# Optimization experiments

Hardware: AMD Instinct MI355X
Metric: run time of the kernel (lower is better)

## Reference

```python
import jax, jax.numpy as jnp
import numpy as np
from functools import partial

T, B, IN, H = 512, 32, 1024, 1024
NUM_LAYERS = 2
SLOPE, OFFSET = 0.2, 0.5
FORGET_GATE_BIAS = 1.0
W_SCALE = 1.0 / np.sqrt(H)  # mimics reset_parameters uniform(-1/sqrt(H), 1/sqrt(H)) scale


def setup_inputs() -> dict:
    key = jax.random.key(0)
    ks = jax.random.split(key, 12)
    x = jax.random.normal(ks[0], (T, B, IN), dtype=jnp.float32)
    h0 = jax.random.normal(ks[1], (NUM_LAYERS, B, H), dtype=jnp.float32)
    c0 = jax.random.normal(ks[2], (NUM_LAYERS, B, H), dtype=jnp.float32)
    def u(k, shape):
        return jax.random.uniform(k, shape, jnp.float32, -W_SCALE, W_SCALE)
    # layer 0: input_size=IN, layer 1: input_size=H
    W_ih0 = u(ks[3], (4 * H, IN))
    W_hh0 = u(ks[4], (4 * H, H))
    b_ih0 = u(ks[5], (4 * H,)).at[H:2 * H].set(FORGET_GATE_BIAS)
    b_hh0 = u(ks[6], (4 * H,)).at[H:2 * H].set(0.0)
    W_ih1 = u(ks[7], (4 * H, H))
    W_hh1 = u(ks[8], (4 * H, H))
    b_ih1 = u(ks[9], (4 * H,)).at[H:2 * H].set(FORGET_GATE_BIAS)
    b_hh1 = u(ks[10], (4 * H,)).at[H:2 * H].set(0.0)
    return {"x": x, "h0": h0, "c0": c0,
            "W_ih0": W_ih0, "W_hh0": W_hh0, "b_ih0": b_ih0, "b_hh0": b_hh0,
            "W_ih1": W_ih1, "W_hh1": W_hh1, "b_ih1": b_ih1, "b_hh1": b_hh1}


def _hard_sigmoid(g):
    return jnp.clip(SLOPE * g + OFFSET, 0.0, 1.0)


def _hardtanh(g):
    return jnp.clip(g, -1.0, 1.0)


def _run_layer(x, h, c, W_ih, W_hh, b_ih, b_hh):
    """HardLSTMLayerForward: per-step eps = mean(x_t) is added to input and state."""
    def step(carry, xt):
        h, c = carry
        eps = jnp.mean(xt)
        xi = xt + eps          # [B, in]
        hh = h + eps           # [B, H]
        cc = c + eps           # [B, H]
        gates = xi @ W_ih.T + b_ih + hh @ W_hh.T + b_hh  # [B, 4H]
        i_g = _hard_sigmoid(gates[:, :H])
        f_g = _hard_sigmoid(gates[:, H:2 * H])
        g_g = _hardtanh(gates[:, 2 * H:3 * H])
        o_g = _hard_sigmoid(gates[:, 3 * H:])
        cy = f_g * cc + i_g * g_g
        hy = o_g * _hardtanh(cy)
        return (hy, cy), hy
    (h, c), y = jax.lax.scan(step, (h, c), x)
    return y, h, c


def reference(x, h0, c0, W_ih0, W_hh0, b_ih0, b_hh0, W_ih1, W_hh1, b_ih1, b_hh1):
    out = x + 1.0  # StackedLSTM adds `one` to the input
    y0, h_0, c_0 = _run_layer(out, h0[0], c0[0], W_ih0, W_hh0, b_ih0, b_hh0)
    y1, h_1, c_1 = _run_layer(y0, h0[1], c0[1], W_ih1, W_hh1, b_ih1, b_hh1)
    hn = jnp.stack([h_0, h_1])  # [num_layers, B, H]
    cn = jnp.stack([c_0, c_1])
    return (y1, hn, cn)
```

## Files before the change

### kernel.cpp

```cpp
#include <hip/hip_runtime.h>
#include <cstdio>


#define T_STEPS 512
#define DEADLINE_TICKS 6000000ULL

typedef __bf16 bf16x8 __attribute__((ext_vector_type(8)));
typedef float  f32x4  __attribute__((ext_vector_type(4)));
typedef unsigned int u32x4 __attribute__((ext_vector_type(4)));
typedef unsigned long long u64;

#define AGLD(p)   __hip_atomic_load((p), __ATOMIC_RELAXED, __HIP_MEMORY_SCOPE_AGENT)
#define AGST(p,v) __hip_atomic_store((p), (v), __ATOMIC_RELAXED, __HIP_MEMORY_SCOPE_AGENT)
#define MFMA16 __builtin_amdgcn_mfma_f32_16x16x32_bf16

__device__ __forceinline__ u64 rtick(){ return __builtin_amdgcn_s_memrealtime(); }

__device__ __forceinline__ unsigned short f2bf(float f){
  union { float f; unsigned u; } v; v.f = f;
  unsigned r = v.u + 0x7FFFu + ((v.u >> 16) & 1u);
  return (unsigned short)(r >> 16);
}
__device__ __forceinline__ bf16x8 packbf(f32x4 a, f32x4 b){
  unsigned u0 = f2bf(a[0]) | ((unsigned)f2bf(a[1])<<16);
  unsigned u1 = f2bf(a[2]) | ((unsigned)f2bf(a[3])<<16);
  unsigned u2 = f2bf(b[0]) | ((unsigned)f2bf(b[1])<<16);
  unsigned u3 = f2bf(b[2]) | ((unsigned)f2bf(b[3])<<16);
  u32x4 cv = {u0,u1,u2,u3};
  return __builtin_bit_cast(bf16x8, cv);
}
__device__ __forceinline__ int fragOff(int row, int k8){
  return ((k8>>2)*2 + (row>>4))*1024 + ((row&15) | ((k8&3)<<4))*16;
}
__device__ __forceinline__ bf16x8 ld_frag_plain(const char* p){
  u32x4 v = *reinterpret_cast<const u32x4*>(p);
  return __builtin_bit_cast(bf16x8, v);
}
__device__ __forceinline__ bf16x8 lds_frag(const char* p){
  u32x4 v = *reinterpret_cast<const u32x4*>(p);
  return __builtin_bit_cast(bf16x8, v);
}

__device__ __forceinline__ void stage64k_c(const char* src, char* dst, int tid){
  const u32x4* s = reinterpret_cast<const u32x4*>(src) + tid;
  u32x4 r0 = s[0],    r1 = s[256],  r2 = s[512],  r3 = s[768];
  u32x4 r4 = s[1024], r5 = s[1280], r6 = s[1536], r7 = s[1792];
  u32x4 r8 = s[2048], r9 = s[2304], ra = s[2560], rb = s[2816];
  u32x4 rc = s[3072], rd = s[3328], re = s[3584], rf = s[3840];
  u32x4* d = (u32x4*)(dst + tid*16);
  d[0]=r0; d[256]=r1; d[512]=r2; d[768]=r3;
  d[1024]=r4; d[1280]=r5; d[1536]=r6; d[1792]=r7;
  d[2048]=r8; d[2304]=r9; d[2560]=ra; d[2816]=rb;
  d[3072]=rc; d[3328]=rd; d[3584]=re; d[3840]=rf;
}
__device__ __forceinline__ void stage64k_b(const char* src, char* dst, int tid){
  u32x4 r0,r1,r2,r3,r4,r5,r6,r7,r8,r9,ra,rb,rc,rd,re,rf;
  u64 a = (u64)(uintptr_t)src + (u64)tid*16;
  #define LD(reg, off) asm volatile("global_load_dwordx4 %0, %1, off sc0 sc1" \
                                    : "=v"(reg) : "v"(a + (off)) : "memory")
  LD(r0,0); LD(r1,4096); LD(r2,8192); LD(r3,12288);
  LD(r4,16384); LD(r5,20480); LD(r6,24576); LD(r7,28672);
  LD(r8,32768); LD(r9,36864); LD(ra,40960); LD(rb,45056);
  LD(rc,49152); LD(rd,53248); LD(re,57344); LD(rf,61440);
  #undef LD
  asm volatile("s_waitcnt vmcnt(0)" ::: "memory");
  u32x4* d = (u32x4*)(dst + tid*16);
  d[0]=r0; d[256]=r1; d[512]=r2; d[768]=r3;
  d[1024]=r4; d[1280]=r5; d[1536]=r6; d[1792]=r7;
  d[2048]=r8; d[2304]=r9; d[2560]=ra; d[2816]=rb;
  d[3072]=rc; d[3328]=rd; d[3584]=re; d[3840]=rf;
}

__device__ __forceinline__ void spin64(const unsigned short* f, unsigned tgt,
                                       int lane, u64 dl){
  if (lane < 8){
    u64 a = (u64)(uintptr_t)f + (u64)lane*16;
    while (true){
      u32x4 v;
      asm volatile("global_load_dwordx4 %0, %1, off sc0 sc1\n\ts_waitcnt vmcnt(0)"
                   : "=v"(v) : "v"(a) : "memory");
      bool ok = true;
      #pragma unroll
      for (int i=0;i<4;++i){
        unsigned u = v[i];
        ok = ok && ((u & 0xFFFFu) >= tgt) && ((u >> 16) >= tgt);
      }
      if (__all((int)ok)) break;
      if (rtick() > dl) break;
    }
  }
  asm volatile("" ::: "memory");
}


__global__ void prep_xfrag(const float* __restrict__ x, unsigned short* __restrict__ xf){
  int tid = blockIdx.x*256 + threadIdx.x;
  int k8 = tid & 127, row = (tid>>7)&31, t = tid>>12;
  const float* s = x + ((size_t)(t*32+row)*1024 + k8*8);
  f32x4 a = *reinterpret_cast<const f32x4*>(s);
  f32x4 b = *reinterpret_cast<const f32x4*>(s+4);
  f32x4 a1 = {a[0]+1.f,a[1]+1.f,a[2]+1.f,a[3]+1.f};
  f32x4 b1 = {b[0]+1.f,b[1]+1.f,b[2]+1.f,b[3]+1.f};
  bf16x8 v = packbf(a1,b1);
  *reinterpret_cast<bf16x8*>((char*)xf + (size_t)t*65536 + fragOff(row,k8)) = v;
}

__global__ void prep_hfrag(const float* __restrict__ h0, unsigned short* __restrict__ hf){
  int tid = blockIdx.x*256 + threadIdx.x;
  int k8 = tid & 127, row = (tid>>7)&31, L = tid>>12;
  const float* s = h0 + ((size_t)(L*32+row)*1024 + k8*8);
  f32x4 a = *reinterpret_cast<const f32x4*>(s);
  f32x4 b = *reinterpret_cast<const f32x4*>(s+4);
  bf16x8 v = packbf(a,b);
  *reinterpret_cast<bf16x8*>((char*)hf + (size_t)L*65536 + fragOff(row,k8)) = v;
}

__global__ void reduce_mean_f32(const float* __restrict__ src, float* __restrict__ out, float add){
  __shared__ float red[256];
  int t = blockIdx.x, tid = threadIdx.x;
  const float* p = src + (size_t)t*32768;
  float s = 0.f;
  for (int i = tid; i < 32768; i += 256) s += p[i];
  red[tid] = s; __syncthreads();
  for (int o = 128; o > 0; o >>= 1){ if (tid < o) red[tid] += red[tid+o]; __syncthreads(); }
  if (tid == 0) out[t] = red[0]*(1.f/32768.f) + add;
}

__global__ void prep_rs(const float* __restrict__ Wih0, const float* __restrict__ Whh0,
                        const float* __restrict__ Wih1, const float* __restrict__ Whh1,
                        const float* __restrict__ bih0, const float* __restrict__ bhh0,
                        const float* __restrict__ bih1, const float* __restrict__ bhh1,
                        float* __restrict__ rs, float* __restrict__ bias){
  int task = blockIdx.x*4 + (threadIdx.x >> 6);
  int lane = threadIdx.x & 63;
  int L = task >> 12, n = task & 4095;
  const float* pi = (L ? Wih1 : Wih0) + (size_t)n*1024;
  const float* ph = (L ? Whh1 : Whh0) + (size_t)n*1024;
  float s = 0.f;
  #pragma unroll
  for (int e = 0; e < 16; ++e){ int k = lane + e*64; s += pi[k] + ph[k]; }
  #pragma unroll
  for (int m = 32; m; m >>= 1) s += __shfl_xor(s, m);
  if (lane == 0){
    rs[task]   = s;
    bias[task] = (L ? bih1[n] : bih0[n]) + (L ? bhh1[n] : bhh0[n]);
  }
}

__global__ __launch_bounds__(256, 1) void rec11(
    const unsigned short* __restrict__ Xf,
    const unsigned short* __restrict__ HiniF,
    unsigned short* __restrict__ Ring0,
    unsigned short* __restrict__ Ring1,
    int ring1mask, int ring1cached,
    float* __restrict__ out,
    const float* __restrict__ Wih0, const float* __restrict__ Whh0,
    const float* __restrict__ Wih1, const float* __restrict__ Whh1,
    const float* __restrict__ biasC, const float* __restrict__ rsC,
    const float* __restrict__ eps0, const float* __restrict__ c0,
    int* __restrict__ epsP,
    unsigned short* __restrict__ flag0,
    unsigned short* __restrict__ flag1)
{
  __shared__ char ldsA[65536];
  __shared__ float ldsPs[4];

  const int tid  = threadIdx.x;
  const int lane = tid & 63;
  const int w    = tid >> 6;
  const int L    = blockIdx.x >> 6;
  const int bid  = blockIdx.x & 63;
  const int jb   = bid * 16;
  const int jc   = jb + w*4;
  const int c    = lane & 15;
  const int q    = c >> 2;
  const int ncol = q*1024 + jc + (c & 3);
  const int koff = (lane >> 4) << 3;
  const u64 dl   = rtick() + DEADLINE_TICKS;

  __builtin_amdgcn_fence(__ATOMIC_ACQUIRE, "agent");
  __syncthreads();

  const float* Wfirst = L ? Whh1 : Wih0;
  const float* Wsec   = L ? Wih1 : Whh0;

  bf16x8 wregF[32], wregS[32];
  {
    const float* sF = Wfirst + (size_t)ncol*1024 + koff;
    const float* sS = Wsec   + (size_t)ncol*1024 + koff;
    #pragma unroll
    for (int kt = 0; kt < 32; ++kt){
      f32x4 a = *reinterpret_cast<const f32x4*>(sF + kt*32);
      f32x4 b = *reinterpret_cast<const f32x4*>(sF + kt*32 + 4);
      wregF[kt] = packbf(a, b);
      f32x4 cc = *reinterpret_cast<const f32x4*>(sS + kt*32);
      f32x4 d  = *reinterpret_cast<const f32x4*>(sS + kt*32 + 4);
      wregS[kt] = packbf(cc, d);
    }
  }

  const float bia = biasC[L*4096 + ncol];
  const float rsv = rsC[L*4096 + ncol];
  const int jw = jc + (c & 3);
  float creg[2][4];
  #pragma unroll
  for (int m = 0; m < 2; ++m)
    #pragma unroll
    for (int r = 0; r < 4; ++r)
      creg[m][r] = c0[L*32768 + (m*16 + (lane>>4)*4 + r)*1024 + jw];

  float* outHn = out + 16777216 + L*32768;
  float* outCn = out + 16777216 + 65536 + L*32768;
  const u64 myFlagA = (u64)(uintptr_t)((L ? flag1 : flag0) + bid);

  for (int t = 0; t < T_STEPS; ++t){
    f32x4 acc0 = {0.f,0.f,0.f,0.f}, acc1 = {0.f,0.f,0.f,0.f};
    float et;

    if (L == 0){
      const char* Ax = (const char*)Xf + (size_t)t*65536;
      #pragma unroll
      for (int kt = 0; kt < 32; ++kt){
        bf16x8 a0 = ld_frag_plain(Ax + (kt*2 + 0)*1024 + lane*16);
        bf16x8 a1 = ld_frag_plain(Ax + (kt*2 + 1)*1024 + lane*16);
        acc0 = MFMA16(a0, wregF[kt], acc0, 0, 0, 0);
        acc1 = MFMA16(a1, wregF[kt], acc1, 0, 0, 0);
      }
      et = eps0[t];
      if (w == 0 && t > 0) spin64(flag0, (unsigned)t, lane, dl);
      __syncthreads();
      const char* hsrc = (t == 0) ? (const char*)HiniF
                                  : (const char*)Ring0 + (size_t)(t-1)*65536;
      stage64k_c(hsrc, ldsA, tid);
      __syncthreads();
      #pragma unroll
      for (int kt = 0; kt < 32; ++kt){
        bf16x8 a0 = lds_frag(ldsA + (kt*2 + 0)*1024 + lane*16);
        bf16x8 a1 = lds_frag(ldsA + (kt*2 + 1)*1024 + lane*16);
        acc0 = MFMA16(a0, wregS[kt], acc0, 0, 0, 0);
        acc1 = MFMA16(a1, wregS[kt], acc1, 0, 0, 0);
      }
    } else {
      if (w == 0 && t > 0) spin64(flag1, (unsigned)t, lane, dl);
      __syncthreads();
      const char* hsrc = (t == 0) ? (const char*)HiniF + 65536
                                  : (const char*)Ring1 + (size_t)((t-1) & ring1mask)*65536;
      if (t == 0 || ring1cached) stage64k_c(hsrc, ldsA, tid);
      else                       stage64k_b(hsrc, ldsA, tid);
      __syncthreads();
      #pragma unroll
      for (int kt = 0; kt < 32; ++kt){
        bf16x8 a0 = lds_frag(ldsA + (kt*2 + 0)*1024 + lane*16);
        bf16x8 a1 = lds_frag(ldsA + (kt*2 + 1)*1024 + lane*16);
        acc0 = MFMA16(a0, wregF[kt], acc0, 0, 0, 0);
        acc1 = MFMA16(a1, wregF[kt], acc1, 0, 0, 0);
      }
      __syncthreads();
      if (w == 0) spin64(flag0, (unsigned)(t+1), lane, dl);
      __syncthreads();
      {
        int s = 0;
        const u64* ep = reinterpret_cast<const u64*>(epsP + (size_t)t*64);
        if (lane < 32){
          u64 v = AGLD(ep + lane);
          s = (int)(unsigned)v + (int)(unsigned)(v >> 32);
        }
        #pragma unroll
        for (int mm = 32; mm; mm >>= 1) s += __shfl_xor(s, mm);
        et = (float)s * 4.6566128730773926e-10f;
      }
      stage64k_c((const char*)Ring0 + (size_t)t*65536, ldsA, tid);
      __syncthreads();
      #pragma unroll
      for (int kt = 0; kt < 32; ++kt){
        bf16x8 a0 = lds_frag(ldsA + (kt*2 + 0)*1024 + lane*16);
        bf16x8 a1 = lds_frag(ldsA + (kt*2 + 1)*1024 + lane*16);
        acc0 = MFMA16(a0, wregS[kt], acc0, 0, 0, 0);
        acc1 = MFMA16(a1, wregS[kt], acc1, 0, 0, 0);
      }
    }

    char* ringSlot = L ? ((char*)Ring1 + (size_t)(t & ring1mask)*65536)
                       : ((char*)Ring0 + (size_t)t*65536);
    float hyv[2][4];
    float psum = 0.f;
    #pragma unroll
    for (int m = 0; m < 2; ++m){
      f32x4 av = m ? acc1 : acc0;
      #pragma unroll
      for (int r = 0; r < 4; ++r){
        float g  = av[r] + bia + et*rsv;
        float p4 = __shfl_xor(g, 4), p8 = __shfl_xor(g, 8), p12 = __shfl_xor(p4, 8);
        float iv = (q==0)?g:(q==1)?p4:(q==2)?p8:p12;
        float fv = (q==1)?g:(q==0)?p4:(q==3)?p8:p12;
        float gv = (q==2)?g:(q==3)?p4:(q==0)?p8:p12;
        float ov = (q==3)?g:(q==2)?p4:(q==1)?p8:p12;
        iv = fminf(fmaxf(0.2f*iv + 0.5f, 0.f), 1.f);
        fv = fminf(fmaxf(0.2f*fv + 0.5f, 0.f), 1.f);
        gv = fminf(fmaxf(gv, -1.f), 1.f);
        ov = fminf(fmaxf(0.2f*ov + 0.5f, 0.f), 1.f);
        float cc = fv*(creg[m][r] + et) + iv*gv;
        creg[m][r] = cc;
        float hy = ov * fminf(fmaxf(cc, -1.f), 1.f);
        hyv[m][r] = hy;
        if (c < 4) psum += hy;

        unsigned short hu = f2bf(hy);
        unsigned p2 = (unsigned)hu | (((unsigned)__shfl_xor((int)hu, 1)) << 16);
        unsigned q2 = (unsigned)__shfl_xor((int)p2, 2);
        if (c == 0){
          int sub = (lane>>4)*4 + r;
          size_t bo = (size_t)((jc>>5)*2 + m)*1024
                    + (size_t)(sub | (((jc>>3)&3)<<4))*16 + (size_t)(jc&7)*2;
          AGST(reinterpret_cast<u64*>(ringSlot + bo), (u64)p2 | ((u64)q2 << 32));
        }
      }
    }
    if (L == 0){
      #pragma unroll
      for (int mm = 32; mm; mm >>= 1) psum += __shfl_xor(psum, mm);
      if (lane == 0) ldsPs[w] = psum;
    }
    asm volatile("s_waitcnt vmcnt(0)" ::: "memory");
    __syncthreads();
    if (tid == 0){
      if (L == 0){
        float bs = ldsPs[0] + ldsPs[1] + ldsPs[2] + ldsPs[3];
        AGST(reinterpret_cast<unsigned*>(epsP + (size_t)t*64 + bid),
             (unsigned)(int)llrintf(bs*65536.f));
        asm volatile("s_waitcnt vmcnt(0)" ::: "memory");
      }
      asm volatile("global_store_short %0, %1, off sc0 sc1"
                   :: "v"(myFlagA), "v"((unsigned)(t+1)) : "memory");
    }

    if (L){
      #pragma unroll
      for (int m = 0; m < 2; ++m)
        #pragma unroll
        for (int r = 0; r < 4; ++r){
          float hy = hyv[m][r];
          float f1 = __shfl_xor(hy, 1), f2 = __shfl_xor(hy, 2), f3 = __shfl_xor(f1, 2);
          if (c == 0){
            int row = m*16 + (lane>>4)*4 + r;
            f32x4 o4 = {hy, f1, f2, f3};
            *reinterpret_cast<f32x4*>(out + (size_t)t*32768 + row*1024 + jc) = o4;
          }
        }
    }
    if (t == T_STEPS-1){
      #pragma unroll
      for (int m = 0; m < 2; ++m)
        #pragma unroll
        for (int r = 0; r < 4; ++r)
          if (c < 4){
            int row = m*16 + (lane>>4)*4 + r;
            outHn[row*1024 + jw] = hyv[m][r];
            outCn[row*1024 + jw] = creg[m][r];
          }
    }
  }
}


extern "C" void kernel_launch(void* const* d_in, const int* in_sizes, int n_in,
                              void* d_out, int out_size, void* d_ws, size_t ws_size,
                              hipStream_t stream)
{
  const float* x    = (const float*)d_in[0];
  const float* h0   = (const float*)d_in[1];
  const float* c0   = (const float*)d_in[2];
  const float* Wih0 = (const float*)d_in[3];
  const float* Whh0 = (const float*)d_in[4];
  const float* bih0 = (const float*)d_in[5];
  const float* bhh0 = (const float*)d_in[6];
  const float* Wih1 = (const float*)d_in[7];
  const float* Whh1 = (const float*)d_in[8];
  const float* bih1 = (const float*)d_in[9];
  const float* bhh1 = (const float*)d_in[10];
  float* out = (float*)d_out;

  char* ws = (char*)d_ws;
  size_t off = 0;
  auto alloc = [&](size_t bytes)->char* {
    char* p = ws + off; off += (bytes + 255) & ~(size_t)255; return p;
  };
  unsigned short* Xf    = (unsigned short*)alloc((size_t)T_STEPS*65536);
  unsigned short* Ring0 = (unsigned short*)alloc((size_t)T_STEPS*65536);
  unsigned short* HiniF = (unsigned short*)alloc(2*65536);
  float* eps0 = (float*)alloc(T_STEPS*4);
  float* bias = (float*)alloc(2*4096*4);
  float* rs   = (float*)alloc(2*4096*4);
  int*   epsP = (int*)alloc((size_t)T_STEPS*64*4);
  char* sync  = alloc(512);
  unsigned short* flag0 = (unsigned short*)sync;
  unsigned short* flag1 = (unsigned short*)(sync + 128);
  size_t remain  = (off <= ws_size) ? (ws_size - off) : 0;
  int r1slots    = (remain >= (size_t)(T_STEPS+1)*65536) ? T_STEPS : 8;
  unsigned short* Ring1 = (unsigned short*)alloc((size_t)r1slots*65536);
  int r1mask   = r1slots - 1;
  int r1cached = (r1slots == T_STEPS) ? 1 : 0;
  if (off > ws_size)
    fprintf(stderr, "HardLSTM: ws too small, need %zu have %zu\n", off, ws_size);

  hipMemsetAsync(sync, 0, 512, stream);
  prep_xfrag<<<8192, 256, 0, stream>>>(x, Xf);
  prep_hfrag<<<32, 256, 0, stream>>>(h0, HiniF);
  reduce_mean_f32<<<T_STEPS, 256, 0, stream>>>(x, eps0, 1.0f);
  prep_rs<<<2048, 256, 0, stream>>>(Wih0, Whh0, Wih1, Whh1,
                                    bih0, bhh0, bih1, bhh1, rs, bias);

  rec11<<<128, 256, 0, stream>>>(Xf, HiniF, Ring0, Ring1, r1mask, r1cached, out,
      Wih0, Whh0, Wih1, Whh1, bias, rs, eps0, c0, epsP, flag0, flag1);
}
```

Before: 6.631 ms.

## Prefetch layer-0 output into second LDS buffer before layer-1 recurrent GEMM

Layer-1 blocks now wait for layer-0's step-t output first, read the eps partials, and stage Ring0[t] into a second 64KB LDS buffer. Only then do they wait on their own recurrent flag. This takes one barrier and spin phase off the critical path between the two GEMM halves. Layer-0 blocks now write per-wave float partial sums straight to global memory instead of reducing them through LDS, which drops one store-and-wait step before the flag publish. The cost is 128KB of LDS per block, and layer 1 blocks earlier on layer 0's progress.

Measured after the change: 6.480 ms. 1.02x faster.

```diff
diff --git a/kernel.cpp b/kernel.cpp
--- a/kernel.cpp
+++ b/kernel.cpp
@@ -147,7 +147,7 @@
   }
 }
 
-__global__ __launch_bounds__(256, 1) void rec11(
+__global__ __launch_bounds__(256, 1) void rec12(
     const unsigned short* __restrict__ Xf,
     const unsigned short* __restrict__ HiniF,
     unsigned short* __restrict__ Ring0,
@@ -158,12 +158,12 @@
     const float* __restrict__ Wih1, const float* __restrict__ Whh1,
     const float* __restrict__ biasC, const float* __restrict__ rsC,
     const float* __restrict__ eps0, const float* __restrict__ c0,
-    int* __restrict__ epsP,
+    unsigned* __restrict__ epsP,
     unsigned short* __restrict__ flag0,
     unsigned short* __restrict__ flag1)
 {
   __shared__ char ldsA[65536];
-  __shared__ float ldsPs[4];
+  __shared__ char ldsB[65536];
 
   const int tid  = threadIdx.x;
   const int lane = tid & 63;
@@ -241,6 +241,21 @@
         acc1 = MFMA16(a1, wregS[kt], acc1, 0, 0, 0);
       }
     } else {
+      if (w == 0) spin64(flag0, (unsigned)(t+1), lane, dl);
+      __syncthreads();
+      {
+        const u64* ep = reinterpret_cast<const u64*>(epsP + (size_t)t*256) + lane*2;
+        u64 v01 = AGLD(ep), v23 = AGLD(ep + 1);
+        union { unsigned u; float f; } w0x,w1x,w2x,w3x;
+        w0x.u = (unsigned)v01; w1x.u = (unsigned)(v01>>32);
+        w2x.u = (unsigned)v23; w3x.u = (unsigned)(v23>>32);
+        float bs = ((w0x.f + w1x.f) + w2x.f) + w3x.f;
+        int s = (int)llrintf(bs * 65536.f);
+        #pragma unroll
+        for (int mm = 32; mm; mm >>= 1) s += __shfl_xor(s, mm);
+        et = (float)s * 4.6566128730773926e-10f;
+      }
+      stage64k_c((const char*)Ring0 + (size_t)t*65536, ldsB, tid);
       if (w == 0 && t > 0) spin64(flag1, (unsigned)t, lane, dl);
       __syncthreads();
       const char* hsrc = (t == 0) ? (const char*)HiniF + 65536
@@ -255,26 +270,10 @@
         acc0 = MFMA16(a0, wregF[kt], acc0, 0, 0, 0);
         acc1 = MFMA16(a1, wregF[kt], acc1, 0, 0, 0);
       }
-      __syncthreads();
-      if (w == 0) spin64(flag0, (unsigned)(t+1), lane, dl);
-      __syncthreads();
-      {
-        int s = 0;
-        const u64* ep = reinterpret_cast<const u64*>(epsP + (size_t)t*64);
-        if (lane < 32){
-          u64 v = AGLD(ep + lane);
-          s = (int)(unsigned)v + (int)(unsigned)(v >> 32);
-        }
-        #pragma unroll
-        for (int mm = 32; mm; mm >>= 1) s += __shfl_xor(s, mm);
-        et = (float)s * 4.6566128730773926e-10f;
-      }
-      stage64k_c((const char*)Ring0 + (size_t)t*65536, ldsA, tid);
-      __syncthreads();
       #pragma unroll
       for (int kt = 0; kt < 32; ++kt){
-        bf16x8 a0 = lds_frag(ldsA + (kt*2 + 0)*1024 + lane*16);
-        bf16x8 a1 = lds_frag(ldsA + (kt*2 + 1)*1024 + lane*16);
+        bf16x8 a0 = lds_frag(ldsB + (kt*2 + 0)*1024 + lane*16);
+        bf16x8 a1 = lds_frag(ldsB + (kt*2 + 1)*1024 + lane*16);
         acc0 = MFMA16(a0, wregS[kt], acc0, 0, 0, 0);
         acc1 = MFMA16(a1, wregS[kt], acc1, 0, 0, 0);
       }
@@ -319,20 +318,16 @@
     if (L == 0){
       #pragma unroll
       for (int mm = 32; mm; mm >>= 1) psum += __shfl_xor(psum, mm);
-      if (lane == 0) ldsPs[w] = psum;
+      if (lane == 0){
+        union { float f; unsigned u; } pb; pb.f = psum;
+        AGST(epsP + (size_t)t*256 + (bid<<2) + w, pb.u);
+      }
     }
     asm volatile("s_waitcnt vmcnt(0)" ::: "memory");
     __syncthreads();
-    if (tid == 0){
-      if (L == 0){
-        float bs = ldsPs[0] + ldsPs[1] + ldsPs[2] + ldsPs[3];
-        AGST(reinterpret_cast<unsigned*>(epsP + (size_t)t*64 + bid),
-             (unsigned)(int)llrintf(bs*65536.f));
-        asm volatile("s_waitcnt vmcnt(0)" ::: "memory");
-      }
+    if (tid == 0)
       asm volatile("global_store_short %0, %1, off sc0 sc1"
                    :: "v"(myFlagA), "v"((unsigned)(t+1)) : "memory");
-    }
 
     if (L){
       #pragma unroll
@@ -391,7 +386,7 @@
   float* eps0 = (float*)alloc(T_STEPS*4);
   float* bias = (float*)alloc(2*4096*4);
   float* rs   = (float*)alloc(2*4096*4);
-  int*   epsP = (int*)alloc((size_t)T_STEPS*64*4);
+  unsigned* epsP = (unsigned*)alloc((size_t)T_STEPS*256*4);
   char* sync  = alloc(512);
   unsigned short* flag0 = (unsigned short*)sync;
   unsigned short* flag1 = (unsigned short*)(sync + 128);
@@ -410,6 +405,6 @@
   prep_rs<<<2048, 256, 0, stream>>>(Wih0, Whh0, Wih1, Whh1,
                                     bih0, bhh0, bih1, bhh1, rs, bias);
 
-  rec11<<<128, 256, 0, stream>>>(Xf, HiniF, Ring0, Ring1, r1mask, r1cached, out,
+  rec12<<<128, 256, 0, stream>>>(Xf, HiniF, Ring0, Ring1, r1mask, r1cached, out,
       Wih0, Whh0, Wih1, Whh1, bias, rs, eps0, c0, epsP, flag0, flag1);
 }
```
